# Kernel tuning notes

Hardware: AMD Instinct MI355X
Metric: run time of the kernel (lower is better)

Reference implementation:

```python
import jax, jax.numpy as jnp
import numpy as np


def setup_inputs() -> dict:
    key = jax.random.key(0)
    ks = jax.random.split(key, 8)
    B, C, H, W = 16, 256, 64, 64
    E, heads, R = 256, 8, 64
    s = 0.02  # small init scale in lieu of xavier
    return {
        "x": jax.random.normal(ks[0], (B, C, H, W), dtype=jnp.float32),
        "Wqkv": jax.random.normal(ks[1], (3 * E, C), dtype=jnp.float32) * s,
        "bqkv": jnp.zeros((3 * E,), dtype=jnp.float32),
        "Wr": jax.random.normal(ks[2], (2 * R * heads, C), dtype=jnp.float32) * s,
        "br": jnp.zeros((2 * R * heads,), dtype=jnp.float32),
        "Wout": jax.random.normal(ks[3], (C, E), dtype=jnp.float32) * s,
        "bout": jnp.zeros((C,), dtype=jnp.float32),
        "alpha": jax.random.normal(ks[4], (1,), dtype=jnp.float32),
        "num_heads": heads,
        "num_regions": R,
    }


def reference(x, Wqkv, bqkv, Wr, br, Wout, bout, alpha, num_heads, num_regions):
    B, C, H, W = x.shape
    N = H * W
    E = Wqkv.shape[0] // 3
    d = E // num_heads  # head_dim
    xf = x.reshape(B, C, N)  # [B, C, N]

    # qkv 1x1 conv -> [B, 3E, N] -> [B, h, N, 3d] -> q,k,v [B, h, N, d]
    qkv = jnp.einsum("oc,bcn->bon", Wqkv, xf) + bqkv[:, None]
    qkv = qkv.reshape(B, num_heads, 3 * d, N).transpose(0, 1, 3, 2)
    q, k, v = jnp.split(qkv, 3, axis=-1)

    # region projections: 1x1 conv + softmax over the FULL channel axis (2*R*heads)
    r = jnp.einsum("oc,bcn->bon", Wr, xf) + br[:, None]
    r = jax.nn.softmax(r, axis=1)
    r = r.reshape(B, num_heads, 2 * num_regions, N).transpose(0, 1, 3, 2)
    Rq, Rk = jnp.split(r, 2, axis=-1)  # each [B, h, N, R]

    # pool tokens into regions: [B, h, d, R]
    qr = jnp.einsum("bhnd,bhnr->bhdr", q, Rq)
    kr = jnp.einsum("bhnd,bhnr->bhdr", k, Rk)
    vr = jnp.einsum("bhnd,bhnr->bhdr", v, Rk)

    # region-level attention [B, h, Rq, Rk], scaled by sqrt(head_dim)
    logits = jnp.einsum("bhdq,bhdk->bhqk", qr, kr) / jnp.sqrt(jnp.asarray(d, x.dtype))
    attn = jax.nn.softmax(logits, axis=-1)  # dropout is identity at eval

    # values = v_r @ attn^T -> [B, h, d, Rq]; expand back to tokens via Rq^T
    vals = jnp.einsum("bhdk,bhqk->bhdq", vr, attn)
    vals = jnp.einsum("bhdq,bhnq->bhdn", vals, Rq)  # [B, h, d, N]

    vals = vals.reshape(B, E, N)
    out = jnp.einsum("oe,ben->bon", Wout, vals) + bout[:, None]
    out = out.reshape(B, C, H, W)
    return x + alpha * out
```

## Files before the change

### kernel.cpp

```cpp
#include <hip/hip_runtime.h>
#include <cstdint>

typedef unsigned short ushort_t;
typedef __attribute__((ext_vector_type(4))) unsigned short ushort4_t;
typedef __attribute__((ext_vector_type(8))) unsigned short ushort8_t;
typedef __attribute__((ext_vector_type(8))) __bf16 bf16x8;
typedef __attribute__((ext_vector_type(4))) float f32x4;

constexpr int NB = 16;
constexpr int NC = 256;
constexpr int NN = 4096;
constexpr int NP = 1024;
constexpr int NT = 512;
constexpr int NO = 768;

static __device__ __forceinline__ ushort_t f2b(float f) {
  uint32_t u = __builtin_bit_cast(uint32_t, f);
  u += 0x7FFFu + ((u >> 16) & 1u);
  return (ushort_t)(u >> 16);
}
static __device__ __forceinline__ float b2f(ushort_t h) {
  return __builtin_bit_cast(float, (uint32_t)h << 16);
}
static __device__ __forceinline__ f32x4 mfma16(bf16x8 a, bf16x8 b, f32x4 c) {
  return __builtin_amdgcn_mfma_f32_16x16x32_bf16(a, b, c, 0, 0, 0);
}
typedef __attribute__((address_space(1))) const unsigned int guint;
typedef __attribute__((address_space(3))) unsigned int luint;
static __device__ __forceinline__ void glds16(const void* g, void* l) {
  __builtin_amdgcn_global_load_lds((guint*)g, (luint*)l, 16, 0, 0);
}

template <int KITERS>
__device__ __forceinline__ void gemm_core(const ushort_t* __restrict__ Asrc, size_t lda,
                                          const ushort_t* __restrict__ Bsrc, size_t ldb,
                                          ushort_t* As, ushort_t* Bs,
                                          f32x4 (&acc)[4][4], int tid) {
  const int l = tid & 63, w = tid >> 6;
  const int fr = l & 15, kq = (l >> 4) * 8;
  const int rr = l >> 3;
  const int sc = ((l & 7) ^ rr) << 3;
  const int swz = (fr & 7) << 3;
  const int wm = (w >> 1) * 64, wn = (w & 1) * 64;
#pragma unroll 1
  for (int it = 0; it < KITERS; it++) {
    const size_t k0 = (size_t)it * 64;
#pragma unroll
    for (int i = 0; i < 4; i++) {
      const int row = i * 32 + w * 8 + rr;
      glds16(Asrc + (size_t)row * lda + k0 + sc, As + (i * 32 + w * 8) * 64);
      glds16(Bsrc + (size_t)row * ldb + k0 + sc, Bs + (i * 32 + w * 8) * 64);
    }
    __syncthreads();
#pragma unroll
    for (int ks = 0; ks < 2; ks++) {
      const int col = ks * 32 + kq;
      bf16x8 af[4], bf[4];
#pragma unroll
      for (int f = 0; f < 4; f++) {
        af[f] = *(const bf16x8*)&As[(wm + f * 16 + fr) * 64 + (col ^ swz)];
        bf[f] = *(const bf16x8*)&Bs[(wn + f * 16 + fr) * 64 + (col ^ swz)];
      }
#pragma unroll
      for (int fm = 0; fm < 4; fm++)
#pragma unroll
        for (int fn = 0; fn < 4; fn++)
          acc[fm][fn] = mfma16(af[fm], bf[fn], acc[fm][fn]);
    }
    __syncthreads();
  }
}

__global__ __launch_bounds__(256) void k0_cvt(const float* __restrict__ x,
                                              ushort_t* __restrict__ xb,
                                              ushort_t* __restrict__ xt) {
  __shared__ ushort_t tr[64][88];
  const int tid = threadIdx.x;
  const int n0 = blockIdx.x * 64, c0 = blockIdx.y * 64, b = blockIdx.z;
  const int cr = (tid >> 4) * 4;
  const int nc4 = (tid & 15) * 4;
#pragma unroll
  for (int i = 0; i < 4; i++) {
    size_t idx = ((size_t)b * NC + c0 + cr + i) * NN + n0 + nc4;
    float4 v = *(const float4*)(x + idx);
    ushort4_t o;
    o[0] = f2b(v.x); o[1] = f2b(v.y); o[2] = f2b(v.z); o[3] = f2b(v.w);
    *(ushort4_t*)(xb + idx) = o;
    tr[nc4 + 0][cr + i] = o[0];
    tr[nc4 + 1][cr + i] = o[1];
    tr[nc4 + 2][cr + i] = o[2];
    tr[nc4 + 3][cr + i] = o[3];
  }
  __syncthreads();
  const int nr = tid >> 2, cc0 = (tid & 3) * 16;
  size_t odx = ((size_t)b * NN + n0 + nr) * NC + c0 + cc0;
  *(ushort8_t*)(xt + odx) = *(const ushort8_t*)&tr[nr][cc0];
  *(ushort8_t*)(xt + odx + 8) = *(const ushort8_t*)&tr[nr][cc0 + 8];
}

__global__ __launch_bounds__(256) void cvt_f2b_k(const float* __restrict__ src,
                                                 ushort_t* __restrict__ dst) {
  int i = (blockIdx.x * 256 + threadIdx.x) * 4;
  float4 v = *(const float4*)(src + i);
  ushort4_t o;
  o[0] = f2b(v.x); o[1] = f2b(v.y); o[2] = f2b(v.z); o[3] = f2b(v.w);
  *(ushort4_t*)(dst + i) = o;
}

__global__ __launch_bounds__(256) void k1_proj(const ushort_t* __restrict__ Wrb,
                                               const ushort_t* __restrict__ xt,
                                               const float* __restrict__ br,
                                               ushort_t* __restrict__ P) {
  __shared__ __align__(16) ushort_t As[128 * 64];
  __shared__ __align__(16) ushort_t Bs[128 * 64];
  const int tid = threadIdx.x;
  const int ord = blockIdx.x;
  const int L = (ord & 7) * 512 + (ord >> 3);
  const int m0 = (L & 7) * 128;
  const int n0 = ((L >> 3) & 31) * 128;
  const int b = L >> 8;
  const int lane = tid & 63, w = tid >> 6;
  const int wm = (w >> 1) * 64, wn = (w & 1) * 64;
  f32x4 acc[4][4] = {};
  gemm_core<4>(Wrb + (size_t)m0 * NC, NC,
               xt + ((size_t)b * NN + n0) * NC, NC, As, Bs, acc, tid);
  const int col = lane & 15, rb = (lane >> 4) * 4;
#pragma unroll
  for (int fm = 0; fm < 4; fm++)
#pragma unroll
    for (int rg = 0; rg < 4; rg++) {
      int row = m0 + wm + fm * 16 + rb + rg;
      float bias = br[row];
#pragma unroll
      for (int fn = 0; fn < 4; fn++) {
        int cc = n0 + wn + fn * 16 + col;
        P[((size_t)b * NP + row) * NN + cc] = f2b(acc[fm][fn][rg] + bias);
      }
    }
}

__global__ __launch_bounds__(512) void k2_softmax(ushort_t* __restrict__ P,
                                                  float* __restrict__ sPpart) {
  __shared__ float red[64][64];
  __shared__ float Mf[64], If[64];
  const int tid = threadIdx.x;
  const int n0 = blockIdx.x * 64, b = blockIdx.y;
  const int cg = tid & 7, pg = tid >> 3;
  ushort_t* base = P + (size_t)b * NP * NN + n0 + cg * 8;

  ushort8_t v[16];
  float m[8];
#pragma unroll
  for (int j = 0; j < 8; j++) m[j] = -3.0e38f;
#pragma unroll
  for (int r = 0; r < 16; r++) {
    v[r] = *(const ushort8_t*)(base + (size_t)(pg * 16 + r) * NN);
#pragma unroll
    for (int j = 0; j < 8; j++) m[j] = fmaxf(m[j], b2f(v[r][j]));
  }
#pragma unroll
  for (int j = 0; j < 8; j++) red[pg][cg * 8 + j] = m[j];
  __syncthreads();
  if (tid < 64) {
    float M = -3.0e38f;
    for (int g = 0; g < 64; g++) M = fmaxf(M, red[g][tid]);
    Mf[tid] = M;
  }
  __syncthreads();
  float mj[8], s[8];
#pragma unroll
  for (int j = 0; j < 8; j++) { mj[j] = Mf[cg * 8 + j]; s[j] = 0.f; }
#pragma unroll
  for (int r = 0; r < 16; r++)
#pragma unroll
    for (int j = 0; j < 8; j++) s[j] += __expf(b2f(v[r][j]) - mj[j]);
#pragma unroll
  for (int j = 0; j < 8; j++) red[pg][cg * 8 + j] = s[j];
  __syncthreads();
  if (tid < 64) {
    float S = 0.f;
    for (int g = 0; g < 64; g++) S += red[g][tid];
    If[tid] = 1.f / S;
  }
  __syncthreads();
  float ij[8];
#pragma unroll
  for (int j = 0; j < 8; j++) ij[j] = If[cg * 8 + j];
#pragma unroll
  for (int r = 0; r < 16; r++) {
    int p = pg * 16 + r;
    ushort8_t o;
    float rs = 0.f;
#pragma unroll
    for (int j = 0; j < 8; j++) {
      float e = __expf(b2f(v[r][j]) - mj[j]) * ij[j];
      o[j] = f2b(e);
      rs += e;
    }
    *(ushort8_t*)(base + (size_t)p * NN) = o;
    rs += __shfl_xor(rs, 1, 64);
    rs += __shfl_xor(rs, 2, 64);
    rs += __shfl_xor(rs, 4, 64);
    if (cg == 0) sPpart[((size_t)blockIdx.x * NB + b) * NP + p] = rs;
  }
}

__global__ __launch_bounds__(256) void k2r_reduce(const float* __restrict__ sPpart,
                                                  float* __restrict__ sP) {
  int idx = blockIdx.x * 256 + threadIdx.x;
  float s = 0.f;
#pragma unroll 8
  for (int bx = 0; bx < 64; bx++) s += sPpart[(size_t)bx * (NB * NP) + idx];
  sP[idx] = s;
}

__global__ __launch_bounds__(256) void k3_pool(const ushort_t* __restrict__ xb,
                                               const ushort_t* __restrict__ P,
                                               float* __restrict__ XR4) {
  __shared__ __align__(16) ushort_t As[128 * 64];
  __shared__ __align__(16) ushort_t Bs[128 * 64];
  const int tid = threadIdx.x;
  const int ord = blockIdx.x;
  const int L = (ord & 7) * 64 + (ord >> 3);
  const int m0 = (L & 1) * 128;
  const int n0 = ((L >> 1) & 7) * 128;
  const int zz = L >> 4;
  const int b = zz >> 1, ks = zz & 1;
  const int lane = tid & 63, w = tid >> 6;
  const int wm = (w >> 1) * 64, wn = (w & 1) * 64;
  f32x4 acc[4][4] = {};
  const size_t kbeg = (size_t)ks * 2048;
  gemm_core<32>(xb + ((size_t)b * NC + m0) * NN + kbeg, NN,
                P + ((size_t)b * NP + n0) * NN + kbeg, NN, As, Bs, acc, tid);
  const int col = lane & 15, rb = (lane >> 4) * 4;
  float* outp = XR4 + (size_t)(ks * NB + b) * NC * NP;
#pragma unroll
  for (int fm = 0; fm < 4; fm++)
#pragma unroll
    for (int fn = 0; fn < 4; fn++)
#pragma unroll
      for (int rg = 0; rg < 4; rg++) {
        int row = m0 + wm + fm * 16 + rb + rg;
        int cc = n0 + wn + fn * 16 + col;
        outp[(size_t)row * NP + cc] = acc[fm][fn][rg];
      }
}

__global__ __launch_bounds__(256) void k3r_tr(const float* __restrict__ XR4,
                                              ushort_t* __restrict__ XRbT) {
  __shared__ ushort_t tr[64][72];
  const int tid = threadIdx.x;
  const int p0 = blockIdx.x * 64, c0 = blockIdx.y * 64, b = blockIdx.z;
  const size_t slice = (size_t)NB * NC * NP;
  const int row = tid >> 4, col4 = (tid & 15) * 4;
#pragma unroll
  for (int i = 0; i < 4; i++) {
    int c = row + i * 16;
    size_t idx = ((size_t)b * NC + c0 + c) * NP + p0 + col4;
    float4 v0 = *(const float4*)(XR4 + idx);
    float4 v1 = *(const float4*)(XR4 + idx + slice);
    tr[col4 + 0][c] = f2b(v0.x + v1.x);
    tr[col4 + 1][c] = f2b(v0.y + v1.y);
    tr[col4 + 2][c] = f2b(v0.z + v1.z);
    tr[col4 + 3][c] = f2b(v0.w + v1.w);
  }
  __syncthreads();
  const int prow = tid >> 2, coff = (tid & 3) * 16;
  size_t odx = ((size_t)b * NP + p0 + prow) * NC + c0 + coff;
  *(ushort8_t*)(XRbT + odx) = *(const ushort8_t*)&tr[prow][coff];
  *(ushort8_t*)(XRbT + odx + 8) = *(const ushort8_t*)&tr[prow][coff + 8];
}

__global__ __launch_bounds__(256) void k4a_qkvr(const ushort_t* __restrict__ Wqkvb,
                                                const ushort_t* __restrict__ XRbT,
                                                const float* __restrict__ bqkv,
                                                const float* __restrict__ sP,
                                                ushort_t* __restrict__ QKVRb) {
  __shared__ __align__(16) ushort_t As[128 * 64];
  __shared__ __align__(16) ushort_t Bs[128 * 64];
  const int tid = threadIdx.x;
  const int ord = blockIdx.x;
  const int L = (ord & 7) * 96 + (ord >> 3);
  const int m0 = (L % 6) * 128;
  const int rest = L / 6;
  const int n0 = (rest & 7) * 128;
  const int b = rest >> 3;
  const int lane = tid & 63, w = tid >> 6;
  const int wm = (w >> 1) * 64, wn = (w & 1) * 64;
  f32x4 acc[4][4] = {};
  gemm_core<4>(Wqkvb + (size_t)m0 * NC, NC,
               XRbT + ((size_t)b * NP + n0) * NC, NC, As, Bs, acc, tid);
  const int col = lane & 15, rb = (lane >> 4) * 4;
  float spv[4];
#pragma unroll
  for (int fn = 0; fn < 4; fn++) spv[fn] = sP[(size_t)b * NP + n0 + wn + fn * 16 + col];
#pragma unroll
  for (int fm = 0; fm < 4; fm++)
#pragma unroll
    for (int rg = 0; rg < 4; rg++) {
      int row = m0 + wm + fm * 16 + rb + rg;
      float bq = bqkv[row];
#pragma unroll
      for (int fn = 0; fn < 4; fn++) {
        int cc = n0 + wn + fn * 16 + col;
        QKVRb[((size_t)b * NO + row) * NP + cc] = f2b(acc[fm][fn][rg] + bq * spv[fn]);
      }
    }
}

__global__ __launch_bounds__(256) void k4b_attn(const ushort_t* __restrict__ QKVRb,
                                                const float* __restrict__ Wout,
                                                ushort_t* __restrict__ Tmb) {
  const int b = blockIdx.x >> 3, h = blockIdx.x & 7;
  const int tid = threadIdx.x;
  __shared__ float qf[96][64];
  __shared__ float attn_sT[64][65];
  __shared__ float vals_s[32][64];
#pragma unroll
  for (int i = 0; i < 3; i++) {
    int u = i * 256 + tid;
    int rw = u >> 3, jc = (u & 7) * 8;
    int p0 = h * 128 + ((rw < 32) ? 0 : 64);
    ushort8_t v = *(const ushort8_t*)(QKVRb + ((size_t)b * NO + h * 96 + rw) * NP + p0 + jc);
#pragma unroll
    for (int j = 0; j < 8; j++) qf[rw][jc + j] = b2f(v[j]);
  }
  __syncthreads();
  const int lj = tid & 63;
  const int rq = tid >> 6;
  float kcol[32];
#pragma unroll
  for (int dd = 0; dd < 32; dd++) kcol[dd] = qf[32 + dd][lj];
  const float isc = 0.17677669529663687f;
#pragma unroll
  for (int r = 0; r < 16; r++) {
    int qi = r * 4 + rq;
    float a = 0.f;
#pragma unroll
    for (int dd = 0; dd < 32; dd++) a += qf[dd][qi] * kcol[dd];
    attn_sT[lj][qi] = a * isc;
  }
  __syncthreads();
  if (tid < 64) {
    float m = -3e38f;
    for (int k = 0; k < 64; k++) m = fmaxf(m, attn_sT[k][tid]);
    float s = 0.f;
    for (int k = 0; k < 64; k++) {
      float e = __expf(attn_sT[k][tid] - m);
      attn_sT[k][tid] = e;
      s += e;
    }
    float inv = 1.f / s;
    for (int k = 0; k < 64; k++) attn_sT[k][tid] *= inv;
  }
  __syncthreads();
  float acol[64];
#pragma unroll
  for (int k = 0; k < 64; k++) acol[k] = attn_sT[k][lj];
#pragma unroll
  for (int r = 0; r < 8; r++) {
    int dd = r * 4 + rq;
    float a = 0.f;
#pragma unroll
    for (int k = 0; k < 64; k++) a += qf[64 + dd][k] * acol[k];
    vals_s[dd][lj] = a;
  }
  __syncthreads();
  float vcol[32];
#pragma unroll
  for (int dd = 0; dd < 32; dd++) vcol[dd] = vals_s[dd][lj];
  for (int r = 0; r < 64; r++) {
    int c = r * 4 + rq;
    const float4* wp = (const float4*)(Wout + (size_t)c * NC + h * 32);
    float a = 0.f;
#pragma unroll
    for (int t = 0; t < 8; t++) {
      float4 w = wp[t];
      a += w.x * vcol[t * 4] + w.y * vcol[t * 4 + 1] + w.z * vcol[t * 4 + 2] +
           w.w * vcol[t * 4 + 3];
    }
    Tmb[((size_t)b * NC + c) * NT + h * 64 + lj] = f2b(a);
  }
}

__global__ __launch_bounds__(256) void k5_out(const float* __restrict__ x,
                                              const ushort_t* __restrict__ P,
                                              const ushort_t* __restrict__ Tmb,
                                              const float* __restrict__ bout,
                                              const float* __restrict__ alpha,
                                              float* __restrict__ out) {
  __shared__ __align__(16) ushort_t As[128 * 64];
  __shared__ __align__(16) ushort_t Bs[128 * 72];
  const int tid = threadIdx.x;
  const int ord = blockIdx.x;
  const int L = (ord & 7) * 128 + (ord >> 3);
  const int m0 = (L & 1) * 128;
  const int n0 = ((L >> 1) & 31) * 128;
  const int b = L >> 6;
  const int lane = tid & 63, w = tid >> 6;
  const int wm = (w >> 1) * 64, wn = (w & 1) * 64;
  const int fr = lane & 15, kq = (lane >> 4) * 8;
  const int rr = lane >> 3, sc = ((lane & 7) ^ rr) << 3;
  const int swz = (fr & 7) << 3;
  const ushort_t* Asrc = Tmb + ((size_t)b * NC + m0) * NT;
  const int kg = tid >> 5, ng = (tid & 31) * 4;
  f32x4 acc[4][4] = {};
  for (int k0 = 0; k0 < NT; k0 += 64) {
#pragma unroll
    for (int i = 0; i < 4; i++) {
      const int row = i * 32 + w * 8 + rr;
      glds16(Asrc + (size_t)row * NT + k0 + sc, As + (i * 32 + w * 8) * 64);
    }
    ushort4_t bv[8];
#pragma unroll
    for (int i = 0; i < 8; i++) {
      int hj = k0 + kg * 8 + i;
      int prow = ((hj >> 6) << 7) + (hj & 63);
      bv[i] = *(const ushort4_t*)(P + ((size_t)b * NP + prow) * NN + n0 + ng);
    }
#pragma unroll
    for (int jj = 0; jj < 4; jj++) {
      ushort8_t pk;
#pragma unroll
      for (int i = 0; i < 8; i++) pk[i] = bv[i][jj];
      *(ushort8_t*)&Bs[(ng + jj) * 72 + kg * 8] = pk;
    }
    __syncthreads();
#pragma unroll
    for (int ks = 0; ks < 2; ks++) {
      const int col = ks * 32 + kq;
      bf16x8 af[4], bf[4];
#pragma unroll
      for (int f = 0; f < 4; f++) {
        af[f] = *(const bf16x8*)&As[(wm + f * 16 + fr) * 64 + (col ^ swz)];
        bf[f] = *(const bf16x8*)&Bs[(wn + f * 16 + fr) * 72 + col];
      }
#pragma unroll
      for (int fm = 0; fm < 4; fm++)
#pragma unroll
        for (int fn = 0; fn < 4; fn++)
          acc[fm][fn] = mfma16(af[fm], bf[fn], acc[fm][fn]);
    }
    __syncthreads();
  }
  const float al = alpha[0];
  const int col = lane & 15, rb = (lane >> 4) * 4;
#pragma unroll
  for (int fm = 0; fm < 4; fm++)
#pragma unroll
    for (int rg = 0; rg < 4; rg++) {
      int row = m0 + wm + fm * 16 + rb + rg;
      float bias = bout[row];
#pragma unroll
      for (int fn = 0; fn < 4; fn++) {
        int cc = n0 + wn + fn * 16 + col;
        size_t idx = ((size_t)b * NC + row) * NN + cc;
        out[idx] = x[idx] + al * (acc[fm][fn][rg] + bias);
      }
    }
}

extern "C" void kernel_launch(void* const* d_in, const int* in_sizes, int n_in,
                              void* d_out, int out_size, void* d_ws, size_t ws_size,
                              hipStream_t stream) {
  const float* x = (const float*)d_in[0];
  const float* Wqkv = (const float*)d_in[1];
  const float* bqkv = (const float*)d_in[2];
  const float* Wr = (const float*)d_in[3];
  const float* br = (const float*)d_in[4];
  const float* Wout = (const float*)d_in[5];
  const float* bout = (const float*)d_in[6];
  const float* alpha = (const float*)d_in[7];
  float* out = (float*)d_out;

  char* ws = (char*)d_ws;
  ushort_t* P = (ushort_t*)ws;
  ushort_t* xb = (ushort_t*)(ws + 134217728);
  ushort_t* XRbT = (ushort_t*)(ws + 134217728);
  ushort_t* xt = (ushort_t*)(ws + 167772160);
  float* XR4 = (float*)(ws + 167772160);
  ushort_t* QKVRb = (ushort_t*)(ws + 167772160);
  ushort_t* Wrb = (ushort_t*)(ws + 201326592);
  float* sPpart = (float*)(ws + 201850880);
  ushort_t* Wqkvb = (ushort_t*)(ws + 201850880);
  float* sP = (float*)(ws + 206045184);
  ushort_t* Tmb = (ushort_t*)(ws + 206110720);

  k0_cvt<<<dim3(64, 4, 16), 256, 0, stream>>>(x, xb, xt);
  cvt_f2b_k<<<256, 256, 0, stream>>>(Wr, Wrb);
  k1_proj<<<4096, 256, 0, stream>>>(Wrb, xt, br, P);
  k2_softmax<<<dim3(64, 16), 512, 0, stream>>>(P, sPpart);
  k2r_reduce<<<64, 256, 0, stream>>>(sPpart, sP);
  cvt_f2b_k<<<192, 256, 0, stream>>>(Wqkv, Wqkvb);
  k3_pool<<<512, 256, 0, stream>>>(xb, P, XR4);
  k3r_tr<<<dim3(16, 4, 16), 256, 0, stream>>>(XR4, XRbT);
  k4a_qkvr<<<768, 256, 0, stream>>>(Wqkvb, XRbT, bqkv, sP, QKVRb);
  k4b_attn<<<128, 256, 0, stream>>>(QKVRb, Wout, Tmb);
  k5_out<<<1024, 256, 0, stream>>>(x, P, Tmb, bout, alpha, out);
}
```

Measured before the change: 337.8 us.

## Double-buffer LDS tiles in GEMM kernels and stage k1 output through shared memory

The shared GEMM core and the output GEMM now use two LDS buffers, so the next K-tile is fetched while MFMAs run on the current one, leaving one barrier per iteration instead of two. The goal is to hide global-load latency behind compute. The projection kernel also writes its bf16 tile into LDS first and then stores it as coalesced 16-byte rows, replacing the scattered 2-byte global writes. In exchange, LDS use per block doubles to 64KB, which can lower occupancy. The global_load_lds into the alternate buffer also depends on the single trailing barrier for correctness.

Measured after the change: 328.1 us. -2.9%, faster.

```diff
diff --git a/kernel.cpp b/kernel.cpp
--- a/kernel.cpp
+++ b/kernel.cpp
@@ -34,32 +34,41 @@
 template <int KITERS>
 __device__ __forceinline__ void gemm_core(const ushort_t* __restrict__ Asrc, size_t lda,
                                           const ushort_t* __restrict__ Bsrc, size_t ldb,
-                                          ushort_t* As, ushort_t* Bs,
-                                          f32x4 (&acc)[4][4], int tid) {
+                                          ushort_t* SH, f32x4 (&acc)[4][4], int tid) {
   const int l = tid & 63, w = tid >> 6;
   const int fr = l & 15, kq = (l >> 4) * 8;
   const int rr = l >> 3;
   const int sc = ((l & 7) ^ rr) << 3;
   const int swz = (fr & 7) << 3;
   const int wm = (w >> 1) * 64, wn = (w & 1) * 64;
+
+  auto STAGE = [&](int bi, size_t k0) {
+    ushort_t* Ad = SH + bi * 8192;
+    ushort_t* Bd = SH + 16384 + bi * 8192;
+#pragma unroll
+    for (int i = 0; i < 4; i++) {
+      const int row = i * 32 + w * 8 + rr;
+      glds16(Asrc + (size_t)row * lda + k0 + sc, Ad + (i * 32 + w * 8) * 64);
+      glds16(Bsrc + (size_t)row * ldb + k0 + sc, Bd + (i * 32 + w * 8) * 64);
+    }
+  };
+
+  STAGE(0, 0);
+  __syncthreads();
+  int cur = 0;
 #pragma unroll 1
   for (int it = 0; it < KITERS; it++) {
-    const size_t k0 = (size_t)it * 64;
-#pragma unroll
-    for (int i = 0; i < 4; i++) {
-      const int row = i * 32 + w * 8 + rr;
-      glds16(Asrc + (size_t)row * lda + k0 + sc, As + (i * 32 + w * 8) * 64);
-      glds16(Bsrc + (size_t)row * ldb + k0 + sc, Bs + (i * 32 + w * 8) * 64);
-    }
-    __syncthreads();
+    if (it + 1 < KITERS) STAGE(cur ^ 1, (size_t)(it + 1) * 64);
+    const ushort_t* Ar = SH + cur * 8192;
+    const ushort_t* Br = SH + 16384 + cur * 8192;
 #pragma unroll
     for (int ks = 0; ks < 2; ks++) {
       const int col = ks * 32 + kq;
       bf16x8 af[4], bf[4];
 #pragma unroll
       for (int f = 0; f < 4; f++) {
-        af[f] = *(const bf16x8*)&As[(wm + f * 16 + fr) * 64 + (col ^ swz)];
-        bf[f] = *(const bf16x8*)&Bs[(wn + f * 16 + fr) * 64 + (col ^ swz)];
+        af[f] = *(const bf16x8*)&Ar[(wm + f * 16 + fr) * 64 + (col ^ swz)];
+        bf[f] = *(const bf16x8*)&Br[(wn + f * 16 + fr) * 64 + (col ^ swz)];
       }
 #pragma unroll
       for (int fm = 0; fm < 4; fm++)
@@ -68,6 +77,7 @@
           acc[fm][fn] = mfma16(af[fm], bf[fn], acc[fm][fn]);
     }
     __syncthreads();
+    cur ^= 1;
   }
 }
 
@@ -111,8 +121,7 @@
                                                const ushort_t* __restrict__ xt,
                                                const float* __restrict__ br,
                                                ushort_t* __restrict__ P) {
-  __shared__ __align__(16) ushort_t As[128 * 64];
-  __shared__ __align__(16) ushort_t Bs[128 * 64];
+  __shared__ __align__(16) ushort_t SH[4 * 8192];
   const int tid = threadIdx.x;
   const int ord = blockIdx.x;
   const int L = (ord & 7) * 512 + (ord >> 3);
@@ -123,20 +132,25 @@
   const int wm = (w >> 1) * 64, wn = (w & 1) * 64;
   f32x4 acc[4][4] = {};
   gemm_core<4>(Wrb + (size_t)m0 * NC, NC,
-               xt + ((size_t)b * NN + n0) * NC, NC, As, Bs, acc, tid);
+               xt + ((size_t)b * NN + n0) * NC, NC, SH, acc, tid);
   const int col = lane & 15, rb = (lane >> 4) * 4;
 #pragma unroll
   for (int fm = 0; fm < 4; fm++)
 #pragma unroll
     for (int rg = 0; rg < 4; rg++) {
-      int row = m0 + wm + fm * 16 + rb + rg;
-      float bias = br[row];
-#pragma unroll
-      for (int fn = 0; fn < 4; fn++) {
-        int cc = n0 + wn + fn * 16 + col;
-        P[((size_t)b * NP + row) * NN + cc] = f2b(acc[fm][fn][rg] + bias);
-      }
-    }
+      int row = wm + fm * 16 + rb + rg;
+      float bias = br[m0 + row];
+#pragma unroll
+      for (int fn = 0; fn < 4; fn++)
+        SH[row * 136 + wn + fn * 16 + col] = f2b(acc[fm][fn][rg] + bias);
+    }
+  __syncthreads();
+  const int orow = tid >> 1, half = tid & 1;
+  const ushort_t* src = &SH[orow * 136 + half * 64];
+  ushort_t* dst = P + ((size_t)b * NP + m0 + orow) * NN + n0 + half * 64;
+#pragma unroll
+  for (int j = 0; j < 8; j++)
+    *(ushort8_t*)(dst + j * 8) = *(const ushort8_t*)(src + j * 8);
 }
 
 __global__ __launch_bounds__(512) void k2_softmax(ushort_t* __restrict__ P,
@@ -217,8 +231,7 @@
 __global__ __launch_bounds__(256) void k3_pool(const ushort_t* __restrict__ xb,
                                                const ushort_t* __restrict__ P,
                                                float* __restrict__ XR4) {
-  __shared__ __align__(16) ushort_t As[128 * 64];
-  __shared__ __align__(16) ushort_t Bs[128 * 64];
+  __shared__ __align__(16) ushort_t SH[4 * 8192];
   const int tid = threadIdx.x;
   const int ord = blockIdx.x;
   const int L = (ord & 7) * 64 + (ord >> 3);
@@ -231,7 +244,7 @@
   f32x4 acc[4][4] = {};
   const size_t kbeg = (size_t)ks * 2048;
   gemm_core<32>(xb + ((size_t)b * NC + m0) * NN + kbeg, NN,
-                P + ((size_t)b * NP + n0) * NN + kbeg, NN, As, Bs, acc, tid);
+                P + ((size_t)b * NP + n0) * NN + kbeg, NN, SH, acc, tid);
   const int col = lane & 15, rb = (lane >> 4) * 4;
   float* outp = XR4 + (size_t)(ks * NB + b) * NC * NP;
 #pragma unroll
@@ -276,8 +289,7 @@
                                                 const float* __restrict__ bqkv,
                                                 const float* __restrict__ sP,
                                                 ushort_t* __restrict__ QKVRb) {
-  __shared__ __align__(16) ushort_t As[128 * 64];
-  __shared__ __align__(16) ushort_t Bs[128 * 64];
+  __shared__ __align__(16) ushort_t SH[4 * 8192];
   const int tid = threadIdx.x;
   const int ord = blockIdx.x;
   const int L = (ord & 7) * 96 + (ord >> 3);
@@ -289,7 +301,7 @@
   const int wm = (w >> 1) * 64, wn = (w & 1) * 64;
   f32x4 acc[4][4] = {};
   gemm_core<4>(Wqkvb + (size_t)m0 * NC, NC,
-               XRbT + ((size_t)b * NP + n0) * NC, NC, As, Bs, acc, tid);
+               XRbT + ((size_t)b * NP + n0) * NC, NC, SH, acc, tid);
   const int col = lane & 15, rb = (lane >> 4) * 4;
   float spv[4];
 #pragma unroll
@@ -389,8 +401,8 @@
                                               const float* __restrict__ bout,
                                               const float* __restrict__ alpha,
                                               float* __restrict__ out) {
-  __shared__ __align__(16) ushort_t As[128 * 64];
-  __shared__ __align__(16) ushort_t Bs[128 * 72];
+  __shared__ __align__(16) ushort_t Ash[2 * 8192];
+  __shared__ __align__(16) ushort_t Bsh[2 * 9216];
   const int tid = threadIdx.x;
   const int ord = blockIdx.x;
   const int L = (ord & 7) * 128 + (ord >> 3);
@@ -405,35 +417,55 @@
   const ushort_t* Asrc = Tmb + ((size_t)b * NC + m0) * NT;
   const int kg = tid >> 5, ng = (tid & 31) * 4;
   f32x4 acc[4][4] = {};
-  for (int k0 = 0; k0 < NT; k0 += 64) {
+  ushort4_t bv[8];
+
+  auto A_STAGE = [&](int bi, int k0) {
+    ushort_t* Ad = Ash + bi * 8192;
 #pragma unroll
     for (int i = 0; i < 4; i++) {
       const int row = i * 32 + w * 8 + rr;
-      glds16(Asrc + (size_t)row * NT + k0 + sc, As + (i * 32 + w * 8) * 64);
-    }
-    ushort4_t bv[8];
+      glds16(Asrc + (size_t)row * NT + k0 + sc, Ad + (i * 32 + w * 8) * 64);
+    }
+  };
+  auto B_LOAD = [&](int k0) {
 #pragma unroll
     for (int i = 0; i < 8; i++) {
       int hj = k0 + kg * 8 + i;
       int prow = ((hj >> 6) << 7) + (hj & 63);
       bv[i] = *(const ushort4_t*)(P + ((size_t)b * NP + prow) * NN + n0 + ng);
     }
+  };
+  auto B_WRITE = [&](int bi) {
 #pragma unroll
     for (int jj = 0; jj < 4; jj++) {
       ushort8_t pk;
 #pragma unroll
       for (int i = 0; i < 8; i++) pk[i] = bv[i][jj];
-      *(ushort8_t*)&Bs[(ng + jj) * 72 + kg * 8] = pk;
-    }
-    __syncthreads();
+      *(ushort8_t*)&Bsh[bi * 9216 + (ng + jj) * 72 + kg * 8] = pk;
+    }
+  };
+
+  A_STAGE(0, 0);
+  B_LOAD(0);
+  B_WRITE(0);
+  __syncthreads();
+  int cur = 0;
+#pragma unroll 1
+  for (int it = 0; it < 8; it++) {
+    if (it + 1 < 8) {
+      A_STAGE(cur ^ 1, (it + 1) * 64);
+      B_LOAD((it + 1) * 64);
+    }
+    const ushort_t* Ar = Ash + cur * 8192;
+    const ushort_t* Br = Bsh + cur * 9216;
 #pragma unroll
     for (int ks = 0; ks < 2; ks++) {
       const int col = ks * 32 + kq;
       bf16x8 af[4], bf[4];
 #pragma unroll
       for (int f = 0; f < 4; f++) {
-        af[f] = *(const bf16x8*)&As[(wm + f * 16 + fr) * 64 + (col ^ swz)];
-        bf[f] = *(const bf16x8*)&Bs[(wn + f * 16 + fr) * 72 + col];
+        af[f] = *(const bf16x8*)&Ar[(wm + f * 16 + fr) * 64 + (col ^ swz)];
+        bf[f] = *(const bf16x8*)&Br[(wn + f * 16 + fr) * 72 + col];
       }
 #pragma unroll
       for (int fm = 0; fm < 4; fm++)
@@ -441,7 +473,9 @@
         for (int fn = 0; fn < 4; fn++)
           acc[fm][fn] = mfma16(af[fm], bf[fn], acc[fm][fn]);
     }
+    if (it + 1 < 8) B_WRITE(cur ^ 1);
     __syncthreads();
+    cur ^= 1;
   }
   const float al = alpha[0];
   const int col = lane & 15, rb = (lane >> 4) * 4;
```
